# Kernel tuning notes

Hardware: AMD Instinct MI355X
Metric: run time of the kernel (lower is better)

Reference implementation:

```python
import jax, jax.numpy as jnp
import numpy as np

B, S, D = 8, 512, 768
H = 12          # attention heads
E = 14          # routed experts
K = 4           # top-k experts per sequence
HID = D * 2     # expert mlp hidden (mlp_ratio=2)
SH = D * 2 * 2  # shared expert hidden (mlp_ratio * n_shared_experts)
EPS = 1e-5


def _ln(x, g, b):
    m = x.mean(-1, keepdims=True)
    v = ((x - m) ** 2).mean(-1, keepdims=True)
    return (x - m) / jnp.sqrt(v + EPS) * g + b


def _gelu(x):
    return jax.nn.gelu(x, approximate=False)


def setup_inputs() -> dict:
    key = jax.random.key(0)
    ks = jax.random.split(key, 12)
    p = lambda k, shape: jax.random.normal(k, shape, jnp.float32) * 0.02
    z = lambda *shape: jnp.zeros(shape, jnp.float32)
    return {
        "x": jax.random.normal(ks[0], (B, S, D), jnp.float32),
        "ln1_g": jnp.ones((D,), jnp.float32), "ln1_b": z(D),
        "qkv_w": p(ks[1], (D, 3 * D)),
        "proj_w": p(ks[2], (D, D)), "proj_b": z(D),
        "ln2_g": jnp.ones((D,), jnp.float32), "ln2_b": z(D),
        "router_w1": p(ks[3], (D, D)), "router_b1": z(D),
        "router_w2": p(ks[4], (D, E)), "router_b2": z(E),
        "exp_w1": p(ks[5], (E, D, HID)), "exp_b1": z(E, HID),
        "exp_w2": p(ks[6], (E, HID, D)), "exp_b2": z(E, D),
        "sh_w1": p(ks[7], (D, SH)), "sh_b1": z(SH),
        "sh_w2": p(ks[8], (SH, D)), "sh_b2": z(D),
    }


def _forward(x, ln1_g, ln1_b, qkv_w, proj_w, proj_b, ln2_g, ln2_b,
             router_w1, router_b1, router_w2, router_b2,
             exp_w1, exp_b1, exp_w2, exp_b2,
             sh_w1, sh_b1, sh_w2, sh_b2):
    dh = D // H
    scale = dh ** -0.5
    # --- attention branch ---
    h1 = _ln(x, ln1_g, ln1_b)
    qkv = (h1 @ qkv_w).reshape(B, S, 3, H, dh)
    q = jnp.moveaxis(qkv[:, :, 0], 2, 1)  # [B,H,S,dh]
    k = jnp.moveaxis(qkv[:, :, 1], 2, 1)
    v = jnp.moveaxis(qkv[:, :, 2], 2, 1)
    att = jax.nn.softmax(jnp.einsum('bhqd,bhkd->bhqk', q, k) * scale, axis=-1)
    ao = jnp.einsum('bhqk,bhkd->bqhd', att, v).reshape(B, S, D) @ proj_w + proj_b
    x2 = x + ao
    # --- MoE branch ---
    h = _ln(x2, ln2_g, ln2_b)
    seq_repr = h.mean(axis=1)                                   # [B,D]
    logits = _gelu(seq_repr @ router_w1 + router_b1) @ router_w2 + router_b2  # [B,E]
    probs = jax.nn.softmax(logits, axis=-1)
    tw, ti = jax.lax.top_k(probs, K)                            # [B,K]
    tw = jax.nn.softmax(tw, axis=-1)                            # re-normalize top-k
    w = (jax.nn.one_hot(ti, E, dtype=tw.dtype) * tw[..., None]).sum(1)  # [B,E]
    # dense all-expert compute; zero weight off the top-k replicates masked routing
    hid = _gelu(jnp.einsum('bsd,edh->ebsh', h, exp_w1) + exp_b1[:, None, None, :])
    eo = jnp.einsum('ebsh,ehd->ebsd', hid, exp_w2) + exp_b2[:, None, None, :]
    y = jnp.einsum('ebsd,be->bsd', eo, w)
    # shared experts
    y = y + _gelu(h @ sh_w1 + sh_b1) @ sh_w2 + sh_b2
    return x2 + y  # ls2 is Identity (init_values=None); aux_loss=0 in eval


def reference(x, ln1_g, ln1_b, qkv_w, proj_w, proj_b, ln2_g, ln2_b,
              router_w1, router_b1, router_w2, router_b2,
              exp_w1, exp_b1, exp_w2, exp_b2,
              sh_w1, sh_b1, sh_w2, sh_b2):
    return _forward(x, ln1_g, ln1_b, qkv_w, proj_w, proj_b, ln2_g, ln2_b,
                    router_w1, router_b1, router_w2, router_b2,
                    exp_w1, exp_b1, exp_w2, exp_b2,
                    sh_w1, sh_b1, sh_w2, sh_b2)
```

## Files before the change

### kernel.cpp

```cpp
#include <hip/hip_runtime.h>
#include <hip/hip_bf16.h>


typedef _Float16 f16x8 __attribute__((ext_vector_type(8)));
typedef _Float16 f16x4 __attribute__((ext_vector_type(4)));
typedef float f32x4 __attribute__((ext_vector_type(4)));
typedef _Float16 f16;

__device__ __forceinline__ float gelu_fast(float x) {
  const float k2l2e = 2.f * 0.7978845608028654f * 1.4426950408889634f;
  float u = (x + 0.044715f * x * x * x) * k2l2e;
  float t = exp2f(u);
  return x * (1.f - 1.f / (t + 1.f));
}

__device__ __forceinline__ f32x4 mfma16(f16x8 a, f16x8 b, f32x4 c) {
  return __builtin_amdgcn_mfma_f32_16x16x32_f16(a, b, c, 0, 0, 0);
}

#define ASYNC_CP16(g, l)                                            \
  __builtin_amdgcn_global_load_lds(                                 \
      (const __attribute__((address_space(1))) void*)(g),           \
      (__attribute__((address_space(3))) void*)(l), 16, 0, 0)

#define GEMM_STAGE(AB, WB, LDA, LDB, koff, buf)                               \
  ASYNC_CP16(&(AB)[(long)fr * (LDA) + (koff) + fc],        &sA[(buf) * 4096 + f]);        \
  ASYNC_CP16(&(AB)[(long)(fr + 64) * (LDA) + (koff) + fc], &sA[(buf) * 4096 + f + 2048]); \
  ASYNC_CP16(&(WB)[(long)fr * (LDB) + (koff) + fc],        &sB[(buf) * 4096 + f]);        \
  ASYNC_CP16(&(WB)[(long)(fr + 64) * (LDB) + (koff) + fc], &sB[(buf) * 4096 + f + 2048]);

#define GEMM_COMPUTE(bufidx)                                                  \
  {                                                                           \
    f16x8 av[4], bv[4];                                                       \
    _Pragma("unroll")                                                         \
    for (int i = 0; i < 4; i++)                                               \
      av[i] = *(const f16x8*)&sA[(bufidx) * 4096 + (wm + i * 16 + lr) * 32 + q4 * 8]; \
    _Pragma("unroll")                                                         \
    for (int j = 0; j < 4; j++)                                               \
      bv[j] = *(const f16x8*)&sB[(bufidx) * 4096 + (wn + j * 16 + lr) * 32 + q4 * 8]; \
    _Pragma("unroll")                                                         \
    for (int i = 0; i < 4; i++)                                               \
      _Pragma("unroll")                                                       \
      for (int j = 0; j < 4; j++) acc[i][j] = mfma16(av[i], bv[j], acc[i][j]); \
  }

#define GEMM_CORE3(AB, WB, LDA, LDB, KK)                                      \
  {                                                                           \
    GEMM_STAGE(AB, WB, LDA, LDB, 0, 0)                                        \
    GEMM_STAGE(AB, WB, LDA, LDB, 32, 1)                                       \
    int cur = 0;                                                              \
    for (int k0 = 0; k0 < (KK); k0 += 32) {                                   \
      if (k0 + 32 < (KK)) {                                                   \
        asm volatile("s_waitcnt vmcnt(4)" ::: "memory");                      \
      } else {                                                                \
        asm volatile("s_waitcnt vmcnt(0)" ::: "memory");                      \
      }                                                                       \
      __builtin_amdgcn_s_barrier();                                           \
      __builtin_amdgcn_sched_barrier(0);                                      \
      if (k0 + 64 < (KK)) {                                                   \
        const int nb = (cur + 2 >= 3) ? cur - 1 : cur + 2;                    \
        GEMM_STAGE(AB, WB, LDA, LDB, k0 + 64, nb)                             \
      }                                                                       \
      GEMM_COMPUTE(cur)                                                       \
      __builtin_amdgcn_sched_barrier(0x38F);                                  \
      cur = (cur == 2) ? 0 : cur + 1;                                         \
    }                                                                         \
  }

#define GEMM_CORE4(AB, WB, LDA, LDB, KK)                                      \
  {                                                                           \
    GEMM_STAGE(AB, WB, LDA, LDB, 0, 0)                                        \
    GEMM_STAGE(AB, WB, LDA, LDB, 32, 1)                                       \
    GEMM_STAGE(AB, WB, LDA, LDB, 64, 2)                                       \
    int cur = 0;                                                              \
    for (int k0 = 0; k0 < (KK); k0 += 32) {                                   \
      if (k0 + 64 < (KK)) {                                                   \
        asm volatile("s_waitcnt vmcnt(8)" ::: "memory");                      \
      } else if (k0 + 32 < (KK)) {                                            \
        asm volatile("s_waitcnt vmcnt(4)" ::: "memory");                      \
      } else {                                                                \
        asm volatile("s_waitcnt vmcnt(0)" ::: "memory");                      \
      }                                                                       \
      __builtin_amdgcn_s_barrier();                                           \
      __builtin_amdgcn_sched_barrier(0);                                      \
      if (k0 + 96 < (KK)) {                                                   \
        const int nb = (cur + 3) & 3;                                         \
        GEMM_STAGE(AB, WB, LDA, LDB, k0 + 96, nb)                             \
      }                                                                       \
      GEMM_COMPUTE(cur)                                                       \
      __builtin_amdgcn_sched_barrier(0x38F);                                  \
      cur = (cur + 1) & 3;                                                    \
    }                                                                         \
  }

__global__ __launch_bounds__(256) void ln_kernel(
    const float* __restrict__ x, const float* __restrict__ g,
    const float* __restrict__ bt, f16* __restrict__ out,
    float* __restrict__ mout, float* __restrict__ rout)
{
  const int row = blockIdx.x;
  const float* xr = x + (long)row * 768;
  const int t = threadIdx.x;
  float v0 = xr[t], v1 = xr[t + 256], v2 = xr[t + 512];
  __shared__ float sb[8];
  float s = v0 + v1 + v2;
  #pragma unroll
  for (int o = 32; o > 0; o >>= 1) s += __shfl_xor(s, o, 64);
  const int w = t >> 6;
  if ((t & 63) == 0) sb[w] = s;
  __syncthreads();
  const float mean = (sb[0] + sb[1] + sb[2] + sb[3]) * (1.0f / 768.0f);
  const float d0 = v0 - mean, d1 = v1 - mean, d2 = v2 - mean;
  float q = d0 * d0 + d1 * d1 + d2 * d2;
  #pragma unroll
  for (int o = 32; o > 0; o >>= 1) q += __shfl_xor(q, o, 64);
  if ((t & 63) == 0) sb[4 + w] = q;
  __syncthreads();
  const float var = (sb[4] + sb[5] + sb[6] + sb[7]) * (1.0f / 768.0f);
  const float rstd = rsqrtf(var + 1e-5f);
  f16* orow = out + (long)row * 768;
  orow[t]       = (f16)(d0 * rstd * g[t]       + bt[t]);
  orow[t + 256] = (f16)(d1 * rstd * g[t + 256] + bt[t + 256]);
  orow[t + 512] = (f16)(d2 * rstd * g[t + 512] + bt[t + 512]);
  if (t == 0) { mout[row] = mean; rout[row] = rstd; }
}

struct TransArgs {
  const float* src[6];
  f16* dst[6];
  int rows[6], cols[6];
  int start[7];
};

__global__ __launch_bounds__(256) void transpose_all(TransArgs ta) {
  const int bid = blockIdx.x;
  int m = 0;
  #pragma unroll
  for (int i = 1; i < 6; i++) if (bid >= ta.start[i]) m = i;
  const int rows = ta.rows[m], cols = ta.cols[m];
  const int tilesC = cols >> 5;
  const int perB = (rows >> 5) * tilesC;
  int local = bid - ta.start[m];
  const int z = local / perB; local -= z * perB;
  const int tr = local / tilesC, tc = local - tr * tilesC;
  const float* inb = ta.src[m] + (long)z * rows * cols;
  f16* outb = ta.dst[m] + (long)z * rows * cols;
  const int c0 = tc * 32, r0 = tr * 32;
  __shared__ float tile[32][33];
  const int tx = threadIdx.x & 31, ty = threadIdx.x >> 5;
  #pragma unroll
  for (int i = 0; i < 32; i += 8)
    tile[ty + i][tx] = inb[(long)(r0 + ty + i) * cols + c0 + tx];
  __syncthreads();
  #pragma unroll
  for (int i = 0; i < 32; i += 8)
    outb[(long)(c0 + ty + i) * rows + r0 + tx] = (f16)tile[tx][ty + i];
}

#define EPI_QKV     0
#define EPI_RESID   1

template <int EPI>
__global__ __launch_bounds__(256) void gemm_bt(
    const f16* __restrict__ A, int K, long strideA, int aShift,
    const f16* __restrict__ W, long strideW,
    const float* __restrict__ bias, int strideBias,
    const int* __restrict__ topkIdx,
    void* __restrict__ outv, long strideOut, int ldout,
    const float* __restrict__ resid)
{
  __shared__ f16 sA[3 * 128 * 32];
  __shared__ f16 sB[3 * 128 * 32];
  const int tid = threadIdx.x;
  const int pair = blockIdx.z;
  const int m0 = blockIdx.y * 128;
  const int n0 = blockIdx.x * 128;
  const f16* Ab = A + ((long)(pair >> aShift)) * strideA + (long)m0 * K;
  const int wsel = topkIdx ? topkIdx[pair] : pair;
  const f16* Wb = W + (long)wsel * strideW + (long)n0 * K;

  const int f = tid * 8;
  const int fr = f >> 5;
  const int fc = f & 31;
  const int lane = tid & 63, wid = tid >> 6;
  const int wm = (wid >> 1) * 64, wn = (wid & 1) * 64;
  const int lr = lane & 15, q4 = lane >> 4;

  f32x4 zero = {0.f, 0.f, 0.f, 0.f};
  f32x4 acc[4][4];
  #pragma unroll
  for (int i = 0; i < 4; i++)
    #pragma unroll
    for (int j = 0; j < 4; j++) acc[i][j] = zero;

  GEMM_CORE3(Ab, Wb, K, K, K);

  #pragma unroll
  for (int i = 0; i < 4; i++) {
    #pragma unroll
    for (int j = 0; j < 4; j++) {
      #pragma unroll
      for (int r = 0; r < 4; r++) {
        const int row = m0 + wm + i * 16 + q4 * 4 + r;
        const int col = n0 + wn + j * 16 + lr;
        float v = acc[i][j][r];
        if constexpr (EPI == EPI_QKV) {
          f16* qb = (f16*)outv;
          const int i3 = col / 768;
          const int rem = col - i3 * 768;
          const int hh = rem >> 6, dd = rem & 63;
          const int bb = row >> 9, ss = row & 511;
          const long bh = bb * 12 + hh;
          if (i3 == 0)      qb[(bh * 512 + ss) * 64 + dd] = (f16)v;
          else if (i3 == 1) qb[3145728 + (bh * 512 + ss) * 64 + dd] = (f16)v;
          else              qb[6291456 + (bh * 64 + dd) * 512 + ss] = (f16)v;
        } else {
          float* ob = (float*)outv;
          v += bias[col];
          ob[(long)row * ldout + col] = resid[(long)row * ldout + col] + v;
        }
      }
    }
  }
}

__global__ __launch_bounds__(256) void gemm_ffn1(
    const f16* __restrict__ hbuf,
    const f16* __restrict__ shw1t, const float* __restrict__ shb1,
    const f16* __restrict__ ew1t,  const float* __restrict__ eb1,
    const int* __restrict__ topk,  const float* __restrict__ wslot,
    f16* __restrict__ shid, f16* __restrict__ hid)
{
  __shared__ f16 smem[4 * 4096 * 2];
  f16* sA = smem;
  f16* sB = smem + 4 * 4096;
  const int orig = blockIdx.x;
  const int xcd = orig & 7, slot = orig >> 3;

  const int tid = threadIdx.x;
  const int f = tid * 8;
  const int fr = f >> 5, fc = f & 31;
  const int lane = tid & 63, wid = tid >> 6;
  const int wm = (wid >> 1) * 64, wn = (wid & 1) * 64;
  const int lr = lane & 15, q4 = lane >> 4;

  const f16* Ab;
  const f16* Wb;
  const float* bp;
  f16* outp;
  int ldo;
  float wscale;

  if (slot < 96) {
    const int l = xcd * 96 + slot;
    const int bx = l % 24, by = l / 24;
    const int n0 = bx * 128, m0 = by * 128;
    Ab = hbuf + (long)m0 * 768;
    Wb = shw1t + (long)n0 * 768;
    bp = shb1 + n0;
    outp = shid + (long)m0 * 3072 + n0;
    ldo = 3072;
    wscale = 1.f;
  } else {
    const int l = xcd * 192 + (slot - 96);
    const int bx = l % 12;
    const int u = l / 12;
    const int by = u & 3, pair = u >> 2;
    const int wsel = topk[pair];
    const int n0 = bx * 128;
    const int m0g = (pair >> 2) * 512 + by * 128;
    Ab = hbuf + (long)m0g * 768;
    Wb = ew1t + (long)wsel * (1536L * 768) + (long)n0 * 768;
    bp = eb1 + (long)wsel * 1536 + n0;
    outp = hid + (long)pair * (512L * 1536) + (long)(by * 128) * 1536 + n0;
    ldo = 1536;
    wscale = wslot[pair];
  }

  f32x4 zero = {0.f, 0.f, 0.f, 0.f};
  f32x4 acc[4][4];
  #pragma unroll
  for (int i = 0; i < 4; i++)
    #pragma unroll
    for (int j = 0; j < 4; j++) acc[i][j] = zero;

  GEMM_CORE4(Ab, Wb, 768, 768, 768);

  __syncthreads();
  #pragma unroll
  for (int i = 0; i < 4; i++)
    #pragma unroll
    for (int j = 0; j < 4; j++)
      #pragma unroll
      for (int r = 0; r < 4; r++) {
        const int rr = wm + i * 16 + q4 * 4 + r;
        const int cc = wn + j * 16 + lr;
        float v = acc[i][j][r] + bp[cc];
        smem[rr * 128 + cc] = (f16)(gelu_fast(v) * wscale);
      }
  __syncthreads();
  {
    const int rsub = tid >> 4;
    const int cseg = (tid & 15) * 8;
    #pragma unroll
    for (int g = 0; g < 8; g++) {
      const int row = g * 16 + rsub;
      *(f16x8*)&outp[(long)row * ldo + cseg] =
          *(const f16x8*)&smem[row * 128 + cseg];
    }
  }
}

__global__ __launch_bounds__(256) void gemm_ffn2(
    const f16* __restrict__ shid, const f16* __restrict__ shw2t,
    const float* __restrict__ shb2, const float* __restrict__ x2,
    const f16* __restrict__ hid, const f16* __restrict__ ew2t,
    const float* __restrict__ eb2,
    const int* __restrict__ topk, const float* __restrict__ wslot,
    float* __restrict__ dout, f16* __restrict__ eo)
{
  __shared__ f16 smem[3 * 4096 * 2];
  f16* sA = smem;
  f16* sB = smem + 3 * 4096;
  const int orig = blockIdx.x;
  const int xcd = orig & 7, slot = orig >> 3;

  const int tid = threadIdx.x;
  const int f = tid * 8;
  const int fr = f >> 5, fc = f & 31;
  const int lane = tid & 63, wid = tid >> 6;
  const int wm = (wid >> 1) * 64, wn = (wid & 1) * 64;
  const int lr = lane & 15, q4 = lane >> 4;

  const bool shared_role = (slot < 24);
  const f16* Ab;
  const f16* Wb;
  int m0, n0, pair = 0, wsel = 0;

  if (shared_role) {
    const int l = xcd * 24 + slot;
    const int bx = l % 6, by = l / 6;
    n0 = bx * 128; m0 = by * 128;
    Ab = shid + (long)m0 * 3072;
    Wb = shw2t + (long)n0 * 3072;
  } else {
    const int l = xcd * 96 + (slot - 24);
    const int bx = l % 6;
    const int u = l / 6;
    const int by = u & 3; pair = u >> 2;
    wsel = topk[pair];
    n0 = bx * 128; m0 = by * 128;
    Ab = hid + (long)pair * (512L * 1536) + (long)m0 * 1536;
    Wb = ew2t + (long)wsel * (768L * 1536) + (long)n0 * 1536;
  }

  f32x4 zero = {0.f, 0.f, 0.f, 0.f};
  f32x4 acc[4][4];
  #pragma unroll
  for (int i = 0; i < 4; i++)
    #pragma unroll
    for (int j = 0; j < 4; j++) acc[i][j] = zero;

  if (shared_role) {
    GEMM_CORE3(Ab, Wb, 3072, 3072, 3072);
  } else {
    GEMM_CORE3(Ab, Wb, 1536, 1536, 1536);
  }

  __syncthreads();
  if (shared_role) {
    float* sf = (float*)smem;
    float* op = dout + (long)m0 * 768 + n0;
    const float* rp = x2 + (long)m0 * 768 + n0;
    const float* bp = shb2 + n0;
    #pragma unroll
    for (int p = 0; p < 2; p++) {
      if ((wid >> 1) == p) {
        #pragma unroll
        for (int i = 0; i < 4; i++)
          #pragma unroll
          for (int j = 0; j < 4; j++)
            #pragma unroll
            for (int r = 0; r < 4; r++)
              sf[(i * 16 + q4 * 4 + r) * 128 + wn + j * 16 + lr] = acc[i][j][r];
      }
      __syncthreads();
      #pragma unroll
      for (int g = 0; g < 8; g++) {
        const int rl = g * 8 + (tid >> 5);
        const int c4 = (tid & 31) * 4;
        const int grow = p * 64 + rl;
        f32x4 v = *(const f32x4*)&sf[rl * 128 + c4];
        const f32x4 rv = *(const f32x4*)&rp[(long)grow * 768 + c4];
        const f32x4 bv = *(const f32x4*)&bp[c4];
        v = v + rv + bv;
        *(f32x4*)&op[(long)grow * 768 + c4] = v;
      }
      __syncthreads();
    }
  } else {
    const float wscale = wslot[pair];
    const float* bp = eb2 + (long)wsel * 768 + n0;
    f16* op = eo + (long)pair * (512L * 768) + (long)m0 * 768 + n0;
    #pragma unroll
    for (int i = 0; i < 4; i++)
      #pragma unroll
      for (int j = 0; j < 4; j++)
        #pragma unroll
        for (int r = 0; r < 4; r++) {
          const int rr = wm + i * 16 + q4 * 4 + r;
          const int cc = wn + j * 16 + lr;
          smem[rr * 128 + cc] = (f16)(acc[i][j][r] + wscale * bp[cc]);
        }
    __syncthreads();
    const int rsub = tid >> 4;
    const int cseg = (tid & 15) * 8;
    #pragma unroll
    for (int g = 0; g < 8; g++) {
      const int row = g * 16 + rsub;
      *(f16x8*)&op[(long)row * 768 + cseg] =
          *(const f16x8*)&smem[row * 128 + cseg];
    }
  }
}

__device__ __forceinline__ int pswz(int row, int col) {
  return row * 512 + (col ^ ((row & 7) << 3));
}

__global__ __launch_bounds__(256) void attn_kernel(
    const f16* __restrict__ Q, const f16* __restrict__ Kt,
    const f16* __restrict__ Vt, f16* __restrict__ AO)
{
  __shared__ f16 Ps[64 * 512];
  const int bh = blockIdx.x;
  const int qt = blockIdx.y;
  const int t = threadIdx.x;
  const int lane = t & 63, w = t >> 6;
  const int lr = lane & 15, q4 = lane >> 4;
  const int r0 = qt * 64 + w * 16;
  const int lrow0 = w * 16;
  const f16* Qh = Q + (long)bh * 512 * 64;
  const f16* Kh = Kt + (long)bh * 512 * 64;

  f32x4 zero = {0.f, 0.f, 0.f, 0.f};
  f32x4 acc[32];
  #pragma unroll
  for (int i = 0; i < 32; i++) acc[i] = zero;

  #pragma unroll
  for (int kk = 0; kk < 2; kk++) {
    f16x8 a = *(const f16x8*)&Qh[(r0 + lr) * 64 + kk * 32 + q4 * 8];
    #pragma unroll
    for (int nt = 0; nt < 32; nt++) {
      f16x8 b = *(const f16x8*)&Kh[(nt * 16 + lr) * 64 + kk * 32 + q4 * 8];
      acc[nt] = mfma16(a, b, acc[nt]);
    }
  }

  const float cscale = 0.125f * 1.44269504089f;
  #pragma unroll
  for (int r = 0; r < 4; r++) {
    float m = -1e30f;
    #pragma unroll
    for (int nt = 0; nt < 32; nt++) m = fmaxf(m, acc[nt][r]);
    #pragma unroll
    for (int o = 1; o < 16; o <<= 1) m = fmaxf(m, __shfl_xor(m, o, 64));
    float s = 0.f;
    #pragma unroll
    for (int nt = 0; nt < 32; nt++) {
      float e = exp2f((acc[nt][r] - m) * cscale);
      acc[nt][r] = e; s += e;
    }
    #pragma unroll
    for (int o = 1; o < 16; o <<= 1) s += __shfl_xor(s, o, 64);
    const float inv = 1.f / s;
    const int lrow = lrow0 + q4 * 4 + r;
    #pragma unroll
    for (int nt = 0; nt < 32; nt++)
      Ps[pswz(lrow, nt * 16 + lr)] = (f16)(acc[nt][r] * inv);
  }

  const f16* Vh = Vt + (long)bh * 64 * 512;
  f32x4 o4[4];
  #pragma unroll
  for (int i = 0; i < 4; i++) o4[i] = zero;
  #pragma unroll
  for (int kk = 0; kk < 16; kk++) {
    f16x8 a = *(const f16x8*)&Ps[pswz(lrow0 + lr, kk * 32 + q4 * 8)];
    #pragma unroll
    for (int nt = 0; nt < 4; nt++) {
      f16x8 b = *(const f16x8*)&Vh[(nt * 16 + lr) * 512 + kk * 32 + q4 * 8];
      o4[nt] = mfma16(a, b, o4[nt]);
    }
  }
  const int b_ = bh / 12, h_ = bh - b_ * 12;
  #pragma unroll
  for (int nt = 0; nt < 4; nt++)
    #pragma unroll
    for (int r = 0; r < 4; r++) {
      const int rowg = r0 + q4 * 4 + r;
      AO[((long)(b_ * 512 + rowg)) * 768 + h_ * 64 + nt * 16 + lr] = (f16)o4[nt][r];
    }
}

__global__ __launch_bounds__(256) void router_reduce(
    const float* __restrict__ x2, const float* __restrict__ lnm,
    const float* __restrict__ lnr, float* __restrict__ part)
{
  const int c = blockIdx.x, b = blockIdx.y, t = threadIdx.x;
  float a0 = 0.f, a1 = 0.f, a2 = 0.f;
  #pragma unroll 4
  for (int s = 0; s < 32; s++) {
    const long base = (long)b * 512 + c * 32 + s;
    const float m = lnm[base], r = lnr[base];
    const float* xr = x2 + base * 768;
    a0 += (xr[t] - m) * r;
    a1 += (xr[t + 256] - m) * r;
    a2 += (xr[t + 512] - m) * r;
  }
  float* pr = part + ((long)b * 16 + c) * 768;
  pr[t] = a0; pr[t + 256] = a1; pr[t + 512] = a2;
}

__global__ __launch_bounds__(256) void router_seq(
    const float* __restrict__ part, const float* __restrict__ g2,
    const float* __restrict__ b2ln, float* __restrict__ seqg)
{
  const int b = blockIdx.x, t = threadIdx.x;
  const float* pb = part + (long)b * 16 * 768;
  #pragma unroll
  for (int i = 0; i < 3; i++) {
    const int j = t + 256 * i;
    float a = 0.f;
    #pragma unroll
    for (int c = 0; c < 16; c++) a += pb[c * 768 + j];
    seqg[b * 768 + j] = a * (1.f / 512.f) * g2[j] + b2ln[j];
  }
}

__global__ __launch_bounds__(256) void router_mlp1(
    const float* __restrict__ seqg, const float* __restrict__ rw1,
    float* __restrict__ pmlp)
{
  const int c = blockIdx.x, b = blockIdx.y, t = threadIdx.x;
  const float* sq = seqg + b * 768 + c * 48;
  float a0 = 0.f, a1 = 0.f, a2 = 0.f;
  #pragma unroll 8
  for (int d = 0; d < 48; d++) {
    const float s = sq[d];
    const float* wr = rw1 + (long)(c * 48 + d) * 768;
    a0 += s * wr[t];
    a1 += s * wr[t + 256];
    a2 += s * wr[t + 512];
  }
  float* pr = pmlp + ((long)b * 16 + c) * 768;
  pr[t] = a0; pr[t + 256] = a1; pr[t + 512] = a2;
}

__global__ __launch_bounds__(256) void router_fold(
    const float* __restrict__ pmlp, const float* __restrict__ rb1,
    float* __restrict__ g1g)
{
  const int b = blockIdx.x, t = threadIdx.x;
  const float* pb = pmlp + (long)b * 16 * 768;
  #pragma unroll
  for (int i = 0; i < 3; i++) {
    const int j = t + 256 * i;
    float a = rb1[j];
    #pragma unroll
    for (int c = 0; c < 16; c++) a += pb[c * 768 + j];
    g1g[b * 768 + j] = 0.5f * a * (1.0f + erff(a * 0.70710678118654752f));
  }
}

__global__ __launch_bounds__(256) void router_top(
    const float* __restrict__ g1g, const float* __restrict__ rw2,
    const float* __restrict__ rb2, float* __restrict__ wslot,
    int* __restrict__ topkIdx)
{
  __shared__ float lg[14];
  const int b = blockIdx.x, t = threadIdx.x;
  const int e = t >> 4, sub = t & 15;
  if (e < 14) {
    float a = 0.f;
    #pragma unroll
    for (int i = 0; i < 48; i++) {
      const int d = sub + 16 * i;
      a += g1g[b * 768 + d] * rw2[d * 14 + e];
    }
    #pragma unroll
    for (int o = 1; o < 16; o <<= 1) a += __shfl_xor(a, o, 64);
    if (sub == 0) lg[e] = a + rb2[e];
  }
  __syncthreads();
  if (t == 0) {
    float mx = -1e30f;
    for (int ee = 0; ee < 14; ee++) mx = fmaxf(mx, lg[ee]);
    float p[14], s = 0.f;
    for (int ee = 0; ee < 14; ee++) { p[ee] = expf(lg[ee] - mx); s += p[ee]; }
    for (int ee = 0; ee < 14; ee++) p[ee] /= s;
    int idx[4]; float val[4]; bool used[14];
    for (int ee = 0; ee < 14; ee++) used[ee] = false;
    for (int k = 0; k < 4; k++) {
      int best = -1; float bv = -1.f;
      for (int ee = 0; ee < 14; ee++)
        if (!used[ee] && p[ee] > bv) { bv = p[ee]; best = ee; }
      used[best] = true; idx[k] = best; val[k] = bv;
    }
    const float m2 = val[0];
    float ss = 0.f, e4[4];
    for (int k = 0; k < 4; k++) { e4[k] = expf(val[k] - m2); ss += e4[k]; }
    for (int k = 0; k < 4; k++) {
      wslot[b * 4 + k] = e4[k] / ss;
      topkIdx[b * 4 + k] = idx[k];
    }
  }
}

__global__ __launch_bounds__(256) void combine_kernel(
    const f16* __restrict__ eo, float* __restrict__ out)
{
  const long i4 = ((long)blockIdx.x * 256 + threadIdx.x) * 4;
  const long b = i4 / (512L * 768);
  const long loc = i4 - b * (512L * 768);
  const f16* e0 = eo + b * 4 * (512L * 768) + loc;
  f32x4 v = *(const f32x4*)&out[i4];
  #pragma unroll
  for (int s = 0; s < 4; s++) {
    const f16x4 ev = *(const f16x4*)&e0[s * (512L * 768)];
    v.x += (float)ev[0];
    v.y += (float)ev[1];
    v.z += (float)ev[2];
    v.w += (float)ev[3];
  }
  *(f32x4*)&out[i4] = v;
}

static const long OFF_X2    = 0L;
static const long OFF_LNM   = 12582912L;
static const long OFF_LNR   = OFF_LNM + 16384L;
static const long OFF_WSLOT = OFF_LNR + 16384L;
static const long OFF_TOPK  = OFF_WSLOT + 256L;
static const long OFF_PART  = OFF_TOPK + 256L;
static const long OFF_SEQG  = OFF_PART + 393216L;
static const long OFF_PMLP  = OFF_SEQG + 24576L;
static const long OFF_G1G   = OFF_PMLP + 393216L;
static const long W_QKVWT  = 13631488L;
static const long W_PROJWT = W_QKVWT + 3538944L;
static const long W_EW1T   = W_PROJWT + 1179648L;
static const long W_EW2T   = W_EW1T + 33030144L;
static const long W_SHW1T  = W_EW2T + 33030144L;
static const long W_SHW2T  = W_SHW1T + 4718592L;
static const long OFF_ACT  = 93847552L;
static const long A_H1     = OFF_ACT;
static const long A_Q      = OFF_ACT + 6291456L;
static const long A_AO     = A_Q + 18874368L;
static const long B_H      = OFF_ACT;
static const long B_HID    = OFF_ACT + 6291456L;
static const long B_SHID   = B_HID + 50331648L;
static const long B_EO     = B_SHID + 25165824L;

extern "C" void kernel_launch(void* const* d_in, const int* in_sizes, int n_in,
                              void* d_out, int out_size, void* d_ws, size_t ws_size,
                              hipStream_t stream) {
  const float* x     = (const float*)d_in[0];
  const float* ln1g  = (const float*)d_in[1];
  const float* ln1b  = (const float*)d_in[2];
  const float* qkvw  = (const float*)d_in[3];
  const float* projw = (const float*)d_in[4];
  const float* projb = (const float*)d_in[5];
  const float* ln2g  = (const float*)d_in[6];
  const float* ln2b  = (const float*)d_in[7];
  const float* rw1   = (const float*)d_in[8];
  const float* rb1   = (const float*)d_in[9];
  const float* rw2   = (const float*)d_in[10];
  const float* rb2   = (const float*)d_in[11];
  const float* ew1   = (const float*)d_in[12];
  const float* eb1   = (const float*)d_in[13];
  const float* ew2   = (const float*)d_in[14];
  const float* eb2   = (const float*)d_in[15];
  const float* shw1  = (const float*)d_in[16];
  const float* shb1  = (const float*)d_in[17];
  const float* shw2  = (const float*)d_in[18];
  const float* shb2  = (const float*)d_in[19];

  char* ws = (char*)d_ws;
  float* x2    = (float*)(ws + OFF_X2);
  float* lnm   = (float*)(ws + OFF_LNM);
  float* lnr   = (float*)(ws + OFF_LNR);
  float* wslot = (float*)(ws + OFF_WSLOT);
  int*   topk  = (int*)(ws + OFF_TOPK);
  float* part  = (float*)(ws + OFF_PART);
  float* seqg  = (float*)(ws + OFF_SEQG);
  float* pmlp  = (float*)(ws + OFF_PMLP);
  float* g1g   = (float*)(ws + OFF_G1G);
  f16* qkvwt  = (f16*)(ws + W_QKVWT);
  f16* projwt = (f16*)(ws + W_PROJWT);
  f16* ew1t   = (f16*)(ws + W_EW1T);
  f16* ew2t   = (f16*)(ws + W_EW2T);
  f16* shw1t  = (f16*)(ws + W_SHW1T);
  f16* shw2t  = (f16*)(ws + W_SHW2T);
  f16* h1     = (f16*)(ws + A_H1);
  f16* Qb     = (f16*)(ws + A_Q);
  f16* aob    = (f16*)(ws + A_AO);
  f16* hbuf   = (f16*)(ws + B_H);
  f16* hid    = (f16*)(ws + B_HID);
  f16* shid   = (f16*)(ws + B_SHID);
  f16* eo     = (f16*)(ws + B_EO);

  TransArgs ta;
  ta.src[0] = qkvw;  ta.dst[0] = qkvwt;  ta.rows[0] = 768;  ta.cols[0] = 2304;
  ta.src[1] = projw; ta.dst[1] = projwt; ta.rows[1] = 768;  ta.cols[1] = 768;
  ta.src[2] = ew1;   ta.dst[2] = ew1t;   ta.rows[2] = 768;  ta.cols[2] = 1536;
  ta.src[3] = ew2;   ta.dst[3] = ew2t;   ta.rows[3] = 1536; ta.cols[3] = 768;
  ta.src[4] = shw1;  ta.dst[4] = shw1t;  ta.rows[4] = 768;  ta.cols[4] = 3072;
  ta.src[5] = shw2;  ta.dst[5] = shw2t;  ta.rows[5] = 3072; ta.cols[5] = 768;
  ta.start[0] = 0;     ta.start[1] = 1728;  ta.start[2] = 2304;
  ta.start[3] = 18432; ta.start[4] = 34560; ta.start[5] = 36864;
  ta.start[6] = 39168;
  transpose_all<<<39168, 256, 0, stream>>>(ta);

  ln_kernel<<<4096, 256, 0, stream>>>(x, ln1g, ln1b, h1, lnm, lnr);
  gemm_bt<EPI_QKV><<<dim3(18, 32, 1), 256, 0, stream>>>(
      h1, 768, 0, 0, qkvwt, 0, nullptr, 0, nullptr, (void*)Qb, 0, 0, nullptr);
  attn_kernel<<<dim3(96, 8, 1), 256, 0, stream>>>(Qb, Qb + 3145728, Qb + 6291456, aob);
  gemm_bt<EPI_RESID><<<dim3(6, 32, 1), 256, 0, stream>>>(
      aob, 768, 0, 0, projwt, 0, projb, 0, nullptr, (void*)x2, 0, 768, x);

  ln_kernel<<<4096, 256, 0, stream>>>(x2, ln2g, ln2b, hbuf, lnm, lnr);
  router_reduce<<<dim3(16, 8, 1), 256, 0, stream>>>(x2, lnm, lnr, part);
  router_seq<<<8, 256, 0, stream>>>(part, ln2g, ln2b, seqg);
  router_mlp1<<<dim3(16, 8, 1), 256, 0, stream>>>(seqg, rw1, pmlp);
  router_fold<<<8, 256, 0, stream>>>(pmlp, rb1, g1g);
  router_top<<<8, 256, 0, stream>>>(g1g, rw2, rb2, wslot, topk);
  gemm_ffn1<<<2304, 256, 0, stream>>>(hbuf, shw1t, shb1, ew1t, eb1,
                                      topk, wslot, shid, hid);
  gemm_ffn2<<<960, 256, 0, stream>>>(shid, shw2t, shb2, x2, hid, ew2t, eb2,
                                     topk, wslot, (float*)d_out, eo);
  combine_kernel<<<3072, 256, 0, stream>>>(eo, (float*)d_out);
}
```

Measured before the change: 568.2 us.

## XOR-swizzle LDS tile layout and drop ffn1 to three-stage pipeline

Applies an XOR swizzle to the 16-byte column chunk of each 32-wide LDS tile row, on both the async global-to-LDS copies and the MFMA fragment reads, to reduce LDS bank conflicts. The ffn1 GEMM also goes from the four-buffer pipeline to the three-buffer one, which cuts its LDS footprint and may allow more resident blocks, at the cost of less prefetch depth. The swizzle must match between writer and reader. The write-side mapping uses tid bits while the read side uses lane bits, so consistency is not guaranteed.

```diff
diff --git a/kernel.cpp b/kernel.cpp
--- a/kernel.cpp
+++ b/kernel.cpp
@@ -24,20 +24,20 @@
       (__attribute__((address_space(3))) void*)(l), 16, 0, 0)
 
 #define GEMM_STAGE(AB, WB, LDA, LDB, koff, buf)                               \
-  ASYNC_CP16(&(AB)[(long)fr * (LDA) + (koff) + fc],        &sA[(buf) * 4096 + f]);        \
-  ASYNC_CP16(&(AB)[(long)(fr + 64) * (LDA) + (koff) + fc], &sA[(buf) * 4096 + f + 2048]); \
-  ASYNC_CP16(&(WB)[(long)fr * (LDB) + (koff) + fc],        &sB[(buf) * 4096 + f]);        \
-  ASYNC_CP16(&(WB)[(long)(fr + 64) * (LDB) + (koff) + fc], &sB[(buf) * 4096 + f + 2048]);
+  ASYNC_CP16(&(AB)[(long)fr * (LDA) + (koff) + fcw],        &sA[(buf) * 4096 + f]);        \
+  ASYNC_CP16(&(AB)[(long)(fr + 64) * (LDA) + (koff) + fcw], &sA[(buf) * 4096 + f + 2048]); \
+  ASYNC_CP16(&(WB)[(long)fr * (LDB) + (koff) + fcw],        &sB[(buf) * 4096 + f]);        \
+  ASYNC_CP16(&(WB)[(long)(fr + 64) * (LDB) + (koff) + fcw], &sB[(buf) * 4096 + f + 2048]);
 
 #define GEMM_COMPUTE(bufidx)                                                  \
   {                                                                           \
     f16x8 av[4], bv[4];                                                       \
     _Pragma("unroll")                                                         \
     for (int i = 0; i < 4; i++)                                               \
-      av[i] = *(const f16x8*)&sA[(bufidx) * 4096 + (wm + i * 16 + lr) * 32 + q4 * 8]; \
+      av[i] = *(const f16x8*)&sA[(bufidx) * 4096 + (wm + i * 16 + lr) * 32 + sv]; \
     _Pragma("unroll")                                                         \
     for (int j = 0; j < 4; j++)                                               \
-      bv[j] = *(const f16x8*)&sB[(bufidx) * 4096 + (wn + j * 16 + lr) * 32 + q4 * 8]; \
+      bv[j] = *(const f16x8*)&sB[(bufidx) * 4096 + (wn + j * 16 + lr) * 32 + sv]; \
     _Pragma("unroll")                                                         \
     for (int i = 0; i < 4; i++)                                               \
       _Pragma("unroll")                                                       \
@@ -67,32 +67,6 @@
     }                                                                         \
   }
 
-#define GEMM_CORE4(AB, WB, LDA, LDB, KK)                                      \
-  {                                                                           \
-    GEMM_STAGE(AB, WB, LDA, LDB, 0, 0)                                        \
-    GEMM_STAGE(AB, WB, LDA, LDB, 32, 1)                                       \
-    GEMM_STAGE(AB, WB, LDA, LDB, 64, 2)                                       \
-    int cur = 0;                                                              \
-    for (int k0 = 0; k0 < (KK); k0 += 32) {                                   \
-      if (k0 + 64 < (KK)) {                                                   \
-        asm volatile("s_waitcnt vmcnt(8)" ::: "memory");                      \
-      } else if (k0 + 32 < (KK)) {                                            \
-        asm volatile("s_waitcnt vmcnt(4)" ::: "memory");                      \
-      } else {                                                                \
-        asm volatile("s_waitcnt vmcnt(0)" ::: "memory");                      \
-      }                                                                       \
-      __builtin_amdgcn_s_barrier();                                           \
-      __builtin_amdgcn_sched_barrier(0);                                      \
-      if (k0 + 96 < (KK)) {                                                   \
-        const int nb = (cur + 3) & 3;                                         \
-        GEMM_STAGE(AB, WB, LDA, LDB, k0 + 96, nb)                             \
-      }                                                                       \
-      GEMM_COMPUTE(cur)                                                       \
-      __builtin_amdgcn_sched_barrier(0x38F);                                  \
-      cur = (cur + 1) & 3;                                                    \
-    }                                                                         \
-  }
-
 __global__ __launch_bounds__(256) void ln_kernel(
     const float* __restrict__ x, const float* __restrict__ g,
     const float* __restrict__ bt, f16* __restrict__ out,
@@ -181,10 +155,11 @@
 
   const int f = tid * 8;
   const int fr = f >> 5;
-  const int fc = f & 31;
+  const int fcw = (((tid & 3) ^ ((tid >> 3) & 3)) * 8);
   const int lane = tid & 63, wid = tid >> 6;
   const int wm = (wid >> 1) * 64, wn = (wid & 1) * 64;
   const int lr = lane & 15, q4 = lane >> 4;
+  const int sv = (q4 ^ ((lr >> 1) & 3)) * 8;
 
   f32x4 zero = {0.f, 0.f, 0.f, 0.f};
   f32x4 acc[4][4];
@@ -231,18 +206,20 @@
     const int* __restrict__ topk,  const float* __restrict__ wslot,
     f16* __restrict__ shid, f16* __restrict__ hid)
 {
-  __shared__ f16 smem[4 * 4096 * 2];
+  __shared__ f16 smem[3 * 4096 * 2];
   f16* sA = smem;
-  f16* sB = smem + 4 * 4096;
+  f16* sB = smem + 3 * 4096;
   const int orig = blockIdx.x;
   const int xcd = orig & 7, slot = orig >> 3;
 
   const int tid = threadIdx.x;
   const int f = tid * 8;
-  const int fr = f >> 5, fc = f & 31;
+  const int fr = f >> 5;
+  const int fcw = (((tid & 3) ^ ((tid >> 3) & 3)) * 8);
   const int lane = tid & 63, wid = tid >> 6;
   const int wm = (wid >> 1) * 64, wn = (wid & 1) * 64;
   const int lr = lane & 15, q4 = lane >> 4;
+  const int sv = (q4 ^ ((lr >> 1) & 3)) * 8;
 
   const f16* Ab;
   const f16* Wb;
@@ -284,7 +261,7 @@
     #pragma unroll
     for (int j = 0; j < 4; j++) acc[i][j] = zero;
 
-  GEMM_CORE4(Ab, Wb, 768, 768, 768);
+  GEMM_CORE3(Ab, Wb, 768, 768, 768);
 
   __syncthreads();
   #pragma unroll
@@ -327,10 +304,12 @@
 
   const int tid = threadIdx.x;
   const int f = tid * 8;
-  const int fr = f >> 5, fc = f & 31;
+  const int fr = f >> 5;
+  const int fcw = (((tid & 3) ^ ((tid >> 3) & 3)) * 8);
   const int lane = tid & 63, wid = tid >> 6;
   const int wm = (wid >> 1) * 64, wn = (wid & 1) * 64;
   const int lr = lane & 15, q4 = lane >> 4;
+  const int sv = (q4 ^ ((lr >> 1) & 3)) * 8;
 
   const bool shared_role = (slot < 24);
   const f16* Ab;
```

New measurement: 565.0 us. No clear change (-0.6%).
